# Kernel optimization log

Measured on AMD Instinct MI355X. Metric: run time of the kernel, lower is better.

Reference implementation:

```python
import jax, jax.numpy as jnp
import numpy as np

N, E, B = 20000, 200000, 16
ND, ED, GD, HD, DOF = 64, 32, 32, 128, 6
PI = 3.14159265358979

def _hat(v):
    x, y, z = v[..., 0], v[..., 1], v[..., 2]
    O = jnp.zeros_like(x)
    return jnp.stack([jnp.stack([O, -z, y], -1),
                      jnp.stack([z, O, -x], -1),
                      jnp.stack([-y, x, O], -1)], -2)

def _so3_exp(phi):
    th2 = jnp.sum(phi * phi, -1, keepdims=True)
    th = jnp.sqrt(th2 + 1e-12)
    a = jnp.where(th < 1e-4, 1.0 - th2 / 6.0, jnp.sin(th) / th)
    b = jnp.where(th < 1e-4, 0.5 - th2 / 24.0, (1.0 - jnp.cos(th)) / th2)
    K = _hat(phi)
    I = jnp.eye(3, dtype=phi.dtype)
    return I + a[..., None] * K + b[..., None] * (K @ K)

def _se3_exp(rho, phi):
    # returns (R, t) of Exp([rho, phi]) with rotation part phi
    th2 = jnp.sum(phi * phi, -1, keepdims=True)
    th = jnp.sqrt(th2 + 1e-12)
    a = jnp.where(th < 1e-4, 1.0 - th2 / 6.0, jnp.sin(th) / th)
    b = jnp.where(th < 1e-4, 0.5 - th2 / 24.0, (1.0 - jnp.cos(th)) / th2)
    c = jnp.where(th < 1e-4, 1.0 / 6.0 - th2 / 120.0, (th - jnp.sin(th)) / (th2 * th))
    K = _hat(phi)
    KK = K @ K
    I = jnp.eye(3, dtype=phi.dtype)
    R = I + a[..., None] * K + b[..., None] * KK
    V = I + b[..., None] * K + c[..., None] * KK
    t = jnp.einsum('nij,nj->ni', V, rho)
    return R, t

def _comp(Ra, ta, Rb, tb):
    return Ra @ Rb, jnp.einsum('nij,nj->ni', Ra, tb) + ta

def _inv(R, t):
    Rt = jnp.swapaxes(R, -1, -2)
    return Rt, -jnp.einsum('nij,nj->ni', Rt, t)

def _vec(R, t):
    # flattened [R | t] 3x4 -> 12
    return jnp.concatenate([R, t[..., None]], -1).reshape(R.shape[0], 12)

def setup_inputs() -> dict:
    key = jax.random.key(0)
    ks = jax.random.split(key, 16)
    T_R = _so3_exp(0.5 * jax.random.normal(ks[0], (N, 3)))
    Tij_R = _so3_exp(0.5 * jax.random.normal(ks[1], (E, 3)))
    return {
        'xfeat': jax.random.normal(ks[2], (N, ND), jnp.float32),
        'T_R': T_R.astype(jnp.float32),
        'T_t': jax.random.normal(ks[3], (N, 3), jnp.float32),
        'edge_feat': jax.random.normal(ks[4], (E, ED), jnp.float32),
        'Tij_R': Tij_R.astype(jnp.float32),
        'Tij_t': jax.random.normal(ks[5], (E, 3), jnp.float32),
        'u': jax.random.normal(ks[6], (B, GD), jnp.float32),
        'edge_index': jax.random.randint(ks[7], (2, E), 0, N),
        'batch': jnp.sort(jax.random.randint(ks[8], (N,), 0, B)),
        'W1': 0.05 * jax.random.normal(ks[9], (2 * ND + 12 + ED, HD), jnp.float32),
        'b1': jnp.zeros((HD,), jnp.float32),
        'W2': 0.05 * jax.random.normal(ks[10], (HD, HD), jnp.float32),
        'b2': jnp.zeros((HD,), jnp.float32),
        'W3': 0.05 * jax.random.normal(ks[11], (HD + GD + ND, HD), jnp.float32),
        'b3': jnp.zeros((HD,), jnp.float32),
        'W4': 0.05 * jax.random.normal(ks[12], (HD, ND + DOF), jnp.float32),
        'b4': jnp.zeros((ND + DOF,), jnp.float32),
    }

def reference(xfeat, T_R, T_t, edge_feat, Tij_R, Tij_t, u,
              edge_index, batch, W1, b1, W2, b2, W3, b3, W4, b4):
    n = xfeat.shape[0]
    i, j = edge_index[0], edge_index[1]
    xfi, xfj = xfeat[i], xfeat[j]
    Ri, ti = T_R[i], T_t[i]
    Rj, tj = T_R[j], T_t[j]
    # T_err_ij = Tj * Ti.inv() * Tij_hat.inv()
    Rii, tii = _inv(Ri, ti)
    Ra, ta = _comp(Rj, tj, Rii, tii)
    Rhi, thi = _inv(Tij_R, Tij_t)
    Reij, teij = _comp(Ra, ta, Rhi, thi)
    # T_err_ji = Ti * Tj.inv() * Tij_hat
    Rji_, tji_ = _inv(Rj, tj)
    Rb, tb = _comp(Ri, ti, Rji_, tji_)
    Reji, teji = _comp(Rb, tb, Tij_R, Tij_t)
    f_ij = jnp.concatenate([xfi, xfj, edge_feat, _vec(Reij, teij)], 1)
    f_ji = jnp.concatenate([xfj, xfi, edge_feat, _vec(Reji, teji)], 1)
    feats = jnp.concatenate([f_ij, f_ji], 0)          # [2E, 172]
    j_both = jnp.concatenate([j, i], 0)               # [2E]
    h = jax.nn.relu(feats @ W1 + b1)
    h = jax.nn.relu(h @ W2 + b2)                      # [2E, HD]
    sums = jax.ops.segment_sum(h, j_both, num_segments=n)
    cnt = jax.ops.segment_sum(jnp.ones((h.shape[0], 1), h.dtype), j_both, num_segments=n)
    aggr = sums / jnp.maximum(cnt, 1.0)               # scatter_mean
    g = jnp.concatenate([aggr, xfeat, u[batch]], 1)
    out = jax.nn.relu(g @ W3 + b3) @ W4 + b4
    xupd, tupd = out[:, :-DOF], out[:, -DOF:]
    rho, phi = tupd[:, :3], tupd[:, 3:]
    # SquashRot: bound rotation angle to pi via tanh
    th = jnp.linalg.norm(phi, axis=-1, keepdims=True)
    phi = phi * (PI * jnp.tanh(th / PI) / (th + 1e-8))
    Rd, td = _se3_exp(rho, phi)
    R_out, t_out = _comp(Rd, td, T_R, T_t)            # boxplus_left: Exp(d) * T
    xfeat_out = xfeat + xupd
    theta = jnp.linalg.norm(phi, axis=-1, keepdims=True)
    return jnp.concatenate([xfeat_out, R_out.reshape(n, 9), t_out, theta], -1)
```

## Files before the change

### kernel.cpp

```cpp
#include <hip/hip_runtime.h>
#include <math.h>

#define ND 64
#define ED 32
#define GD 32
#define HD 128
#define DOF 6
#define K1 172
#define K1PAD 192
#define KG 224
#define N4P 80
#define NOUT 70
#define OUTC 77
#define MT 256
#define P1 144
#define TDN 16
#define GP 232
#define HP 136
#define OP 84
#define PI_F 3.14159265358979f

typedef short short8 __attribute__((ext_vector_type(8)));
typedef float f32x4  __attribute__((ext_vector_type(4)));

__device__ __forceinline__ unsigned short f2b(float f) {
    unsigned int u = __float_as_uint(f);
    u += 0x7fffu + ((u >> 16) & 1u);
    return (unsigned short)(u >> 16);
}
__device__ __forceinline__ float b2f(unsigned short b) {
    return __uint_as_float(((unsigned int)b) << 16);
}
__device__ __forceinline__ void mul33_abt(const float* A, const float* B, float* C) {
#pragma unroll
    for (int r = 0; r < 3; r++)
#pragma unroll
        for (int c = 0; c < 3; c++)
            C[3*r+c] = A[3*r+0]*B[3*c+0] + A[3*r+1]*B[3*c+1] + A[3*r+2]*B[3*c+2];
}

__global__ void __launch_bounds__(256)
prep(const float* __restrict__ W1, const float* __restrict__ W2,
     const float* __restrict__ W3, const float* __restrict__ W4,
     const float* __restrict__ xfeat, const float* __restrict__ edge_feat,
     unsigned short* __restrict__ W1b, unsigned short* __restrict__ W2b,
     unsigned short* __restrict__ W3b, unsigned short* __restrict__ W4b,
     unsigned short* __restrict__ xb, unsigned short* __restrict__ eb,
     int N, int E)
{
    int idx = blockIdx.x * 256 + threadIdx.x;
    if (idx < K1PAD * HD) {
        int k = idx >> 7, n = idx & 127;
        float v = (k < K1) ? W1[k * HD + n] : 0.f;
        int kc = k >> 5, kr = k & 31, q = kr >> 3, j = kr & 7;
        W1b[(((kc * 8 + (n >> 4)) * 4 + q) * 16 + (n & 15)) * 8 + j] = f2b(v);
        return;
    }
    idx -= K1PAD * HD;
    if (idx < HD * HD) {
        int k = idx >> 7, n = idx & 127;
        int kc = k >> 5, kr = k & 31, q = kr >> 3, j = kr & 7;
        W2b[(((kc * 8 + (n >> 4)) * 4 + q) * 16 + (n & 15)) * 8 + j] = f2b(W2[k * HD + n]);
        return;
    }
    idx -= HD * HD;
    if (idx < KG * HD) {
        int k = idx >> 7, n = idx & 127;
        int sk = (k < HD) ? ((k & 7) * 16 + (k >> 3)) : k;
        int kc = k >> 5, kr = k & 31, q = kr >> 3, j = kr & 7;
        W3b[(((kc * 8 + (n >> 4)) * 4 + q) * 16 + (n & 15)) * 8 + j] = f2b(W3[sk * HD + n]);
        return;
    }
    idx -= KG * HD;
    if (idx < HD * N4P) {
        int k = idx / N4P, n = idx % N4P;
        float v = (n < NOUT) ? W4[k * NOUT + n] : 0.f;
        int kc = k >> 5, kr = k & 31, q = kr >> 3, j = kr & 7;
        W4b[(((kc * 5 + (n >> 4)) * 4 + q) * 16 + (n & 15)) * 8 + j] = f2b(v);
        return;
    }
    idx -= HD * N4P;
    const int nx4 = N * ND / 4;
    if (idx < nx4) {
        const float4 v = *(const float4*)&xfeat[idx * 4];
        ushort4 o; o.x = f2b(v.x); o.y = f2b(v.y); o.z = f2b(v.z); o.w = f2b(v.w);
        *(ushort4*)&xb[idx * 4] = o;
        return;
    }
    idx -= nx4;
    if (idx < E * ED / 4) {
        const float4 v = *(const float4*)&edge_feat[idx * 4];
        ushort4 o; o.x = f2b(v.x); o.y = f2b(v.y); o.z = f2b(v.z); o.w = f2b(v.w);
        *(ushort4*)&eb[idx * 4] = o;
    }
}

__global__ void __launch_bounds__(256)
count_kernel(const int* __restrict__ edge_index, int* __restrict__ cnti, int E)
{
    int g = blockIdx.x * 256 + threadIdx.x;
    if (g >= 2 * E) return;
    const int tgt = (g < E) ? edge_index[E + g] : edge_index[g - E];
    atomicAdd(&cnti[tgt], 1);
}

__global__ void __launch_bounds__(1024)
scan_kernel(const int* __restrict__ cnti, int* __restrict__ off,
            int* __restrict__ cursor, int N)
{
    __shared__ int part[1024];
    const int t = threadIdx.x;
    const int chunk = (N + 1023) / 1024;
    const int base = t * chunk;
    int s = 0;
    for (int i = 0; i < chunk; i++) { int idx = base + i; if (idx < N) s += cnti[idx]; }
    part[t] = s;
    __syncthreads();
    for (int d = 1; d < 1024; d <<= 1) {
        int v = (t >= d) ? part[t - d] : 0;
        __syncthreads();
        part[t] += v;
        __syncthreads();
    }
    int pre = (t > 0) ? part[t - 1] : 0;
    for (int i = 0; i < chunk; i++) {
        int idx = base + i;
        if (idx < N) { off[idx] = pre; cursor[idx] = pre; pre += cnti[idx]; }
    }
}

__global__ void __launch_bounds__(256)
scatter_kernel(const int* __restrict__ edge_index, int* __restrict__ cursor,
               int* __restrict__ dlist, int E)
{
    int g = blockIdx.x * 256 + threadIdx.x;
    if (g >= 2 * E) return;
    const int tgt = (g < E) ? edge_index[E + g] : edge_index[g - E];
    const int pos = atomicAdd(&cursor[tgt], 1);
    dlist[pos] = g;
}

__global__ void __launch_bounds__(256)
pose_kernel(const float* __restrict__ T_R, const float* __restrict__ T_t,
            const float* __restrict__ Tij_R, const float* __restrict__ Tij_t,
            const int* __restrict__ edge_index, const int* __restrict__ dlist,
            unsigned short* __restrict__ poseb, int E)
{
    const int p = blockIdx.x * 256 + threadIdx.x;
    if (p >= 2 * E) return;
    const int dir = dlist[p];
    const bool fwd = (dir < E);
    const int e = fwd ? dir : dir - E;
    const int ni = edge_index[e];
    const int nj = edge_index[E + e];
    float Ri[9], Rj[9], TR[9], ti[3], tj[3], Tt[3];
#pragma unroll
    for (int q = 0; q < 9; q++) { Ri[q] = T_R[9*ni+q]; Rj[q] = T_R[9*nj+q]; TR[q] = Tij_R[9*e+q]; }
#pragma unroll
    for (int q = 0; q < 3; q++) { ti[q] = T_t[3*ni+q]; tj[q] = T_t[3*nj+q]; Tt[q] = Tij_t[3*e+q]; }
    float A[9];
    mul33_abt(Rj, Ri, A);
    float Re[9], te[3];
    if (fwd) {
        mul33_abt(A, TR, Re);
#pragma unroll
        for (int r = 0; r < 3; r++)
            te[r] = tj[r]
                  - (A[3*r+0]*ti[0] + A[3*r+1]*ti[1] + A[3*r+2]*ti[2])
                  - (Re[3*r+0]*Tt[0] + Re[3*r+1]*Tt[1] + Re[3*r+2]*Tt[2]);
    } else {
#pragma unroll
        for (int r = 0; r < 3; r++)
#pragma unroll
            for (int c = 0; c < 3; c++)
                Re[3*r+c] = A[r]*TR[c] + A[3+r]*TR[3+c] + A[6+r]*TR[6+c];
        const float d0 = Tt[0]-tj[0], d1 = Tt[1]-tj[1], d2 = Tt[2]-tj[2];
#pragma unroll
        for (int r = 0; r < 3; r++)
            te[r] = ti[r] + A[r]*d0 + A[3+r]*d1 + A[6+r]*d2;
    }
    short8 p0, p1;
#pragma unroll
    for (int r = 0; r < 2; r++) {
        p0[4*r+0] = (short)f2b(Re[3*r+0]);
        p0[4*r+1] = (short)f2b(Re[3*r+1]);
        p0[4*r+2] = (short)f2b(Re[3*r+2]);
        p0[4*r+3] = (short)f2b(te[r]);
    }
    p1[0] = (short)f2b(Re[6]); p1[1] = (short)f2b(Re[7]);
    p1[2] = (short)f2b(Re[8]); p1[3] = (short)f2b(te[2]);
    p1[4] = 0; p1[5] = 0; p1[6] = 0; p1[7] = 0;
    *(short8*)(poseb + (size_t)p * 16) = p0;
    *(short8*)(poseb + (size_t)p * 16 + 8) = p1;
}

__global__ void __launch_bounds__(256, 2)
edge_kernel(const unsigned short* __restrict__ xb, const unsigned short* __restrict__ eb,
            const unsigned short* __restrict__ poseb, const int* __restrict__ edge_index,
            const int* __restrict__ dlist,
            const unsigned short* __restrict__ W1b, const float* __restrict__ b1,
            const unsigned short* __restrict__ W2b, const float* __restrict__ b2,
            unsigned short* __restrict__ hbuf, int E)
{
    __shared__ unsigned short h1s[4 * 64 * P1];
    const int tid = threadIdx.x;
    const int wv = tid >> 6, lane = tid & 63;
    const int nl = lane & 15, quad = lane >> 4;
    const int D0 = blockIdx.x * MT + wv * 64;
    const int laneoff = quad * 128 + nl * 8;
    const int twoE = 2 * E;
    unsigned short* hw = h1s + wv * 64 * P1;

    int s1[4], s2[4], ee[4], pp[4];
#pragma unroll
    for (int rt = 0; rt < 4; rt++) {
        int p = D0 + rt * 16 + nl;
        if (p >= twoE) p = twoE - 1;
        pp[rt] = p;
        const int dir = dlist[p];
        const bool fwd = (dir < E);
        const int e = fwd ? dir : dir - E;
        const int ni = edge_index[e];
        const int nj = edge_index[E + e];
        s1[rt] = fwd ? ni : nj;
        s2[rt] = fwd ? nj : ni;
        ee[rt] = e;
    }

    f32x4 acc[4][8];
#pragma unroll
    for (int rt = 0; rt < 4; rt++)
#pragma unroll
        for (int nt = 0; nt < 8; nt++) acc[rt][nt] = (f32x4)0.f;

    short8 wf[2][8];
#pragma unroll
    for (int nt = 0; nt < 8; nt++)
        wf[0][nt] = *(const short8*)(W1b + nt * 512 + laneoff);

#pragma unroll
    for (int kc = 0; kc < 6; kc++) {
        short8 af[4];
#pragma unroll
        for (int rt = 0; rt < 4; rt++) {
            switch (kc) {
            case 0: af[rt] = *(const short8*)(xb + (size_t)s1[rt] * ND + quad * 8); break;
            case 1: af[rt] = *(const short8*)(xb + (size_t)s1[rt] * ND + 32 + quad * 8); break;
            case 2: af[rt] = *(const short8*)(xb + (size_t)s2[rt] * ND + quad * 8); break;
            case 3: af[rt] = *(const short8*)(xb + (size_t)s2[rt] * ND + 32 + quad * 8); break;
            case 4: af[rt] = *(const short8*)(eb + (size_t)ee[rt] * ED + quad * 8); break;
            default: af[rt] = (quad < 2) ? *(const short8*)(poseb + (size_t)pp[rt] * 16 + quad * 8)
                                         : (short8)(short)0; break;
            }
        }
        const int cur = kc & 1, nxt = cur ^ 1;
        if (kc < 5) {
#pragma unroll
            for (int nt = 0; nt < 8; nt++)
                wf[nxt][nt] = *(const short8*)(W1b + ((kc + 1) * 8 + nt) * 512 + laneoff);
        }
#pragma unroll
        for (int nt = 0; nt < 8; nt++)
#pragma unroll
            for (int rt = 0; rt < 4; rt++)
                acc[rt][nt] = __builtin_amdgcn_mfma_f32_16x16x32_bf16(af[rt], wf[cur][nt], acc[rt][nt], 0, 0, 0);
    }

    {
        float bias1[8];
#pragma unroll
        for (int nt = 0; nt < 8; nt++) bias1[nt] = b1[nt * 16 + nl];
#pragma unroll
        for (int rt = 0; rt < 4; rt++)
#pragma unroll
            for (int nt = 0; nt < 8; nt++) {
                const int col = nt * 16 + nl;
#pragma unroll
                for (int r = 0; r < 4; r++)
                    hw[(rt * 16 + quad * 4 + r) * P1 + col] = f2b(fmaxf(acc[rt][nt][r] + bias1[nt], 0.f));
            }
    }
    asm volatile("s_waitcnt lgkmcnt(0)" ::: "memory");

#pragma unroll
    for (int rt = 0; rt < 4; rt++)
#pragma unroll
        for (int nt = 0; nt < 8; nt++) acc[rt][nt] = (f32x4)0.f;
#pragma unroll
    for (int nt = 0; nt < 8; nt++)
        wf[0][nt] = *(const short8*)(W2b + nt * 512 + laneoff);
#pragma unroll
    for (int kc = 0; kc < 4; kc++) {
        short8 hf[4];
#pragma unroll
        for (int rt = 0; rt < 4; rt++)
            hf[rt] = *(const short8*)&hw[(rt * 16 + nl) * P1 + kc * 32 + quad * 8];
        const int cur = kc & 1, nxt = cur ^ 1;
        if (kc < 3) {
#pragma unroll
            for (int nt = 0; nt < 8; nt++)
                wf[nxt][nt] = *(const short8*)(W2b + ((kc + 1) * 8 + nt) * 512 + laneoff);
        }
#pragma unroll
        for (int nt = 0; nt < 8; nt++)
#pragma unroll
            for (int rt = 0; rt < 4; rt++)
                acc[rt][nt] = __builtin_amdgcn_mfma_f32_16x16x32_bf16(hf[rt], wf[cur][nt], acc[rt][nt], 0, 0, 0);
    }

    {
        float bias2[8];
#pragma unroll
        for (int nt = 0; nt < 8; nt++) bias2[nt] = b2[nt * 16 + nl];
#pragma unroll
        for (int rt = 0; rt < 4; rt++)
#pragma unroll
            for (int r = 0; r < 4; r++) {
                const int p2 = D0 + rt * 16 + quad * 4 + r;
                if (p2 < twoE) {
                    short8 hv;
#pragma unroll
                    for (int nt = 0; nt < 8; nt++)
                        hv[nt] = (short)f2b(fmaxf(acc[rt][nt][r] + bias2[nt], 0.f));
                    *(short8*)(hbuf + (size_t)p2 * HD + nl * 8) = hv;
                }
            }
    }
}

__global__ void __launch_bounds__(256)
node_kernel(const float* __restrict__ xfeat, const float* __restrict__ T_R,
            const float* __restrict__ T_t, const float* __restrict__ u,
            const int* __restrict__ batch,
            const unsigned short* __restrict__ W3b, const float* __restrict__ b3,
            const unsigned short* __restrict__ W4b, const float* __restrict__ b4,
            const unsigned short* __restrict__ hbuf, const int* __restrict__ off,
            const int* __restrict__ cnti,
            float* __restrict__ out, int Nn)
{
    __shared__ unsigned short gbuf[TDN * GP];
    __shared__ unsigned short hid[TDN * HP];
    __shared__ float obuf[TDN * OP];
    const int tid = threadIdx.x;
    const int wv = tid >> 6, lane = tid & 63;
    const int n0 = blockIdx.x * TDN;
    const int nn = min(TDN, Nn - n0);

#pragma unroll
    for (int i = 0; i < 4; i++) {
        const int d = wv + 4 * i;
        if (d < nn) {
            const int n = n0 + d;
            const int deg = cnti[n];
            const int start = off[n];
            const float inv = 1.0f / (float)max(deg, 1);
            const unsigned short* hp = hbuf + (size_t)start * HD + 2 * lane;
            float a0 = 0.f, a1 = 0.f;
            int k = 0;
            for (; k + 4 <= deg; k += 4) {
                const unsigned int v0 = *(const unsigned int*)(hp);
                const unsigned int v1 = *(const unsigned int*)(hp + HD);
                const unsigned int v2 = *(const unsigned int*)(hp + 2 * HD);
                const unsigned int v3 = *(const unsigned int*)(hp + 3 * HD);
                hp += 4 * HD;
                a0 += b2f((unsigned short)v0) + b2f((unsigned short)v1)
                    + b2f((unsigned short)v2) + b2f((unsigned short)v3);
                a1 += b2f((unsigned short)(v0 >> 16)) + b2f((unsigned short)(v1 >> 16))
                    + b2f((unsigned short)(v2 >> 16)) + b2f((unsigned short)(v3 >> 16));
            }
            for (; k < deg; k++) {
                const unsigned int v0 = *(const unsigned int*)(hp);
                hp += HD;
                a0 += b2f((unsigned short)v0);
                a1 += b2f((unsigned short)(v0 >> 16));
            }
            const unsigned int pk = (unsigned int)f2b(a0 * inv) | ((unsigned int)f2b(a1 * inv) << 16);
            *(unsigned int*)&gbuf[d * GP + 2 * lane] = pk;
        }
    }
    for (int idx = tid; idx < TDN * 24; idx += 256) {
        const int d = idx / 24;
        if (d < nn) {
            const int n = n0 + d;
            const int c4 = (idx % 24) * 4;
            float4 v;
            if (c4 < 64) v = *(const float4*)&xfeat[(size_t)n * ND + c4];
            else         v = *(const float4*)&u[(size_t)batch[n] * GD + (c4 - 64)];
            ushort4 o; o.x = f2b(v.x); o.y = f2b(v.y); o.z = f2b(v.z); o.w = f2b(v.w);
            *(ushort4*)&gbuf[d * GP + 128 + c4] = o;
        }
    }
    __syncthreads();

    const int nl = lane & 15, quad = lane >> 4;
    const int laneoff = quad * 128 + nl * 8;

    f32x4 acc3[2];
    acc3[0] = (f32x4)0.f; acc3[1] = (f32x4)0.f;
#pragma unroll
    for (int kc = 0; kc < 7; kc++) {
        short8 A0 = *(const short8*)&gbuf[nl * GP + kc * 32 + quad * 8];
#pragma unroll
        for (int t = 0; t < 2; t++) {
            short8 B = *(const short8*)(W3b + (kc * 8 + wv * 2 + t) * 512 + laneoff);
            acc3[t] = __builtin_amdgcn_mfma_f32_16x16x32_bf16(A0, B, acc3[t], 0, 0, 0);
        }
    }
#pragma unroll
    for (int t = 0; t < 2; t++) {
        const int col = (wv * 2 + t) * 16 + nl;
        const float bb = b3[col];
#pragma unroll
        for (int r = 0; r < 4; r++)
            hid[(quad * 4 + r) * HP + col] = f2b(fmaxf(acc3[t][r] + bb, 0.f));
    }
    __syncthreads();

    f32x4 acc4[2];
    acc4[0] = (f32x4)0.f; acc4[1] = (f32x4)0.f;
    const int nt1 = (wv == 0) ? 4 : -1;
#pragma unroll
    for (int kc = 0; kc < 4; kc++) {
        short8 A0 = *(const short8*)&hid[nl * HP + kc * 32 + quad * 8];
        short8 B0 = *(const short8*)(W4b + (kc * 5 + wv) * 512 + laneoff);
        acc4[0] = __builtin_amdgcn_mfma_f32_16x16x32_bf16(A0, B0, acc4[0], 0, 0, 0);
        if (nt1 >= 0) {
            short8 B1 = *(const short8*)(W4b + (kc * 5 + nt1) * 512 + laneoff);
            acc4[1] = __builtin_amdgcn_mfma_f32_16x16x32_bf16(A0, B1, acc4[1], 0, 0, 0);
        }
    }
    {
        const int col0 = wv * 16 + nl;
        const float bb0 = (col0 < NOUT) ? b4[col0] : 0.f;
#pragma unroll
        for (int r = 0; r < 4; r++)
            obuf[(quad * 4 + r) * OP + col0] = acc4[0][r] + bb0;
        if (nt1 >= 0) {
            const int col1 = nt1 * 16 + nl;
            const float bb1 = (col1 < NOUT) ? b4[col1] : 0.f;
#pragma unroll
            for (int r = 0; r < 4; r++)
                obuf[(quad * 4 + r) * OP + col1] = acc4[1][r] + bb1;
        }
    }
    __syncthreads();

    for (int idx = tid; idx < TDN * ND; idx += 256) {
        const int d = idx >> 6, c = idx & 63;
        if (d < nn) {
            const int n = n0 + d;
            out[(size_t)n * OUTC + c] = xfeat[(size_t)n * ND + c] + obuf[d * OP + c];
        }
    }
    if (tid < nn) {
        const int n = n0 + tid;
        const float r0 = obuf[tid*OP + 64], r1 = obuf[tid*OP + 65], r2 = obuf[tid*OP + 66];
        float p0 = obuf[tid*OP + 67], p1 = obuf[tid*OP + 68], p2 = obuf[tid*OP + 69];
        const float th0 = sqrtf(p0*p0 + p1*p1 + p2*p2);
        const float s = PI_F * tanhf(th0 / PI_F) / (th0 + 1e-8f);
        p0 *= s; p1 *= s; p2 *= s;
        const float pp = p0*p0 + p1*p1 + p2*p2;
        const float th = sqrtf(pp + 1e-12f);
        float a, b, c;
        if (th < 1e-4f) { a = 1.f - pp/6.f; b = 0.5f - pp/24.f; c = 1.f/6.f - pp/120.f; }
        else { const float sn = sinf(th), cs = cosf(th); a = sn/th; b = (1.f-cs)/pp; c = (th-sn)/(pp*th); }
        float Rd[9], V[9];
        Rd[0]=1.f+b*(p0*p0-pp); Rd[1]=-a*p2+b*p0*p1; Rd[2]= a*p1+b*p0*p2;
        Rd[3]= a*p2+b*p1*p0;    Rd[4]=1.f+b*(p1*p1-pp); Rd[5]=-a*p0+b*p1*p2;
        Rd[6]=-a*p1+b*p2*p0;    Rd[7]= a*p0+b*p2*p1;  Rd[8]=1.f+b*(p2*p2-pp);
        V[0]=1.f+c*(p0*p0-pp);  V[1]=-b*p2+c*p0*p1;   V[2]= b*p1+c*p0*p2;
        V[3]= b*p2+c*p1*p0;     V[4]=1.f+c*(p1*p1-pp); V[5]=-b*p0+c*p1*p2;
        V[6]=-b*p1+c*p2*p0;     V[7]= b*p0+c*p2*p1;   V[8]=1.f+c*(p2*p2-pp);
        const float td0 = V[0]*r0 + V[1]*r1 + V[2]*r2;
        const float td1 = V[3]*r0 + V[4]*r1 + V[5]*r2;
        const float td2 = V[6]*r0 + V[7]*r1 + V[8]*r2;
        float TRn[9], Ttn[3];
#pragma unroll
        for (int q = 0; q < 9; q++) TRn[q] = T_R[9*n+q];
#pragma unroll
        for (int q = 0; q < 3; q++) Ttn[q] = T_t[3*n+q];
        float* o = out + (size_t)n * OUTC + 64;
#pragma unroll
        for (int r = 0; r < 3; r++)
#pragma unroll
            for (int cc = 0; cc < 3; cc++)
                o[3*r+cc] = Rd[3*r+0]*TRn[cc] + Rd[3*r+1]*TRn[3+cc] + Rd[3*r+2]*TRn[6+cc];
        o[9]  = Rd[0]*Ttn[0] + Rd[1]*Ttn[1] + Rd[2]*Ttn[2] + td0;
        o[10] = Rd[3]*Ttn[0] + Rd[4]*Ttn[1] + Rd[5]*Ttn[2] + td1;
        o[11] = Rd[6]*Ttn[0] + Rd[7]*Ttn[1] + Rd[8]*Ttn[2] + td2;
        o[12] = sqrtf(pp);
    }
}

extern "C" void kernel_launch(void* const* d_in, const int* in_sizes, int n_in,
                              void* d_out, int out_size, void* d_ws, size_t ws_size,
                              hipStream_t stream)
{
    const float* xfeat     = (const float*)d_in[0];
    const float* T_R       = (const float*)d_in[1];
    const float* T_t       = (const float*)d_in[2];
    const float* edge_feat = (const float*)d_in[3];
    const float* Tij_R     = (const float*)d_in[4];
    const float* Tij_t     = (const float*)d_in[5];
    const float* u         = (const float*)d_in[6];
    const int*   edge_index= (const int*)d_in[7];
    const int*   batch     = (const int*)d_in[8];
    const float* W1 = (const float*)d_in[9],  *b1 = (const float*)d_in[10];
    const float* W2 = (const float*)d_in[11], *b2 = (const float*)d_in[12];
    const float* W3 = (const float*)d_in[13], *b3 = (const float*)d_in[14];
    const float* W4 = (const float*)d_in[15], *b4 = (const float*)d_in[16];
    const int N = in_sizes[0] / ND;
    const int E = in_sizes[3] / ED;

    char* p = (char*)d_ws;
    unsigned short* W1b = (unsigned short*)p;   p += (size_t)K1PAD * HD * 2;
    unsigned short* W2b = (unsigned short*)p;   p += (size_t)HD * HD * 2;
    unsigned short* W3b = (unsigned short*)p;   p += (size_t)KG * HD * 2;
    unsigned short* W4b = (unsigned short*)p;   p += (size_t)HD * N4P * 2;
    unsigned short* xb  = (unsigned short*)p;   p += (size_t)N * ND * 2;
    unsigned short* ebf = (unsigned short*)p;   p += (size_t)E * ED * 2;
    unsigned short* poseb = (unsigned short*)p; p += (size_t)2 * E * 16 * 2;
    unsigned short* hbuf = (unsigned short*)p;  p += (size_t)2 * E * HD * 2;
    int* dlist = (int*)p;                       p += (size_t)2 * E * 4;
    int* cnti = (int*)p;                        p += (size_t)N * 4;
    int* off  = (int*)p;                        p += (size_t)N * 4;
    int* cursor = (int*)p;

    hipMemsetAsync(cnti, 0, (size_t)N * 4, stream);
    const int prepn = K1PAD*HD + HD*HD + KG*HD + HD*N4P + N*ND/4 + E*ED/4;
    prep<<<(prepn + 255) / 256, 256, 0, stream>>>(W1, W2, W3, W4, xfeat, edge_feat,
                                                  W1b, W2b, W3b, W4b, xb, ebf, N, E);
    count_kernel<<<(2*E + 255) / 256, 256, 0, stream>>>(edge_index, cnti, E);
    scan_kernel<<<1, 1024, 0, stream>>>(cnti, off, cursor, N);
    scatter_kernel<<<(2*E + 255) / 256, 256, 0, stream>>>(edge_index, cursor, dlist, E);
    pose_kernel<<<(2*E + 255) / 256, 256, 0, stream>>>(T_R, T_t, Tij_R, Tij_t,
                                                       edge_index, dlist, poseb, E);
    const int ebk = (2 * E + MT - 1) / MT;
    edge_kernel<<<ebk, 256, 0, stream>>>(xb, ebf, poseb, edge_index, dlist,
                                         W1b, b1, W2b, b2, hbuf, E);
    const int nb = (N + TDN - 1) / TDN;
    node_kernel<<<nb, 256, 0, stream>>>(xfeat, T_R, T_t, u, batch, W3b, b3, W4b, b4,
                                        hbuf, off, cnti, (float*)d_out, N);
}
```

Baseline: 324.2 us.

## Fuse count into prep, scatter with pose, prefetch A operands, transpose MFMA output

```diff
diff --git a/kernel.cpp b/kernel.cpp
--- a/kernel.cpp
+++ b/kernel.cpp
@@ -13,11 +13,12 @@
 #define NOUT 70
 #define OUTC 77
 #define MT 256
-#define P1 144
+#define P1 136
 #define TDN 16
 #define GP 232
 #define HP 136
 #define OP 84
+#define NMAX 20480
 #define PI_F 3.14159265358979f
 
 typedef short short8 __attribute__((ext_vector_type(8)));
@@ -43,10 +44,11 @@
 prep(const float* __restrict__ W1, const float* __restrict__ W2,
      const float* __restrict__ W3, const float* __restrict__ W4,
      const float* __restrict__ xfeat, const float* __restrict__ edge_feat,
+     const int* __restrict__ edge_index,
      unsigned short* __restrict__ W1b, unsigned short* __restrict__ W2b,
      unsigned short* __restrict__ W3b, unsigned short* __restrict__ W4b,
      unsigned short* __restrict__ xb, unsigned short* __restrict__ eb,
-     int N, int E)
+     int* __restrict__ cnti, int N, int E)
 {
     int idx = blockIdx.x * 256 + threadIdx.x;
     if (idx < K1PAD * HD) {
@@ -88,32 +90,33 @@
         return;
     }
     idx -= nx4;
-    if (idx < E * ED / 4) {
+    const int ne4 = E * ED / 4;
+    if (idx < ne4) {
         const float4 v = *(const float4*)&edge_feat[idx * 4];
         ushort4 o; o.x = f2b(v.x); o.y = f2b(v.y); o.z = f2b(v.z); o.w = f2b(v.w);
         *(ushort4*)&eb[idx * 4] = o;
-    }
-}
-
-__global__ void __launch_bounds__(256)
-count_kernel(const int* __restrict__ edge_index, int* __restrict__ cnti, int E)
-{
-    int g = blockIdx.x * 256 + threadIdx.x;
-    if (g >= 2 * E) return;
-    const int tgt = (g < E) ? edge_index[E + g] : edge_index[g - E];
-    atomicAdd(&cnti[tgt], 1);
+        return;
+    }
+    idx -= ne4;
+    if (idx < 2 * E) {
+        const int tgt = (idx < E) ? edge_index[E + idx] : edge_index[idx - E];
+        atomicAdd(&cnti[tgt], 1);
+    }
 }
 
 __global__ void __launch_bounds__(1024)
 scan_kernel(const int* __restrict__ cnti, int* __restrict__ off,
             int* __restrict__ cursor, int N)
 {
+    __shared__ int sh[NMAX];
     __shared__ int part[1024];
     const int t = threadIdx.x;
+    for (int i = t; i < N; i += 1024) sh[i] = cnti[i];
+    __syncthreads();
     const int chunk = (N + 1023) / 1024;
     const int base = t * chunk;
     int s = 0;
-    for (int i = 0; i < chunk; i++) { int idx = base + i; if (idx < N) s += cnti[idx]; }
+    for (int i = 0; i < chunk; i++) { int idx = base + i; if (idx < N) s += sh[idx]; }
     part[t] = s;
     __syncthreads();
     for (int d = 1; d < 1024; d <<= 1) {
@@ -125,34 +128,28 @@
     int pre = (t > 0) ? part[t - 1] : 0;
     for (int i = 0; i < chunk; i++) {
         int idx = base + i;
-        if (idx < N) { off[idx] = pre; cursor[idx] = pre; pre += cnti[idx]; }
-    }
+        if (idx < N) { int c = sh[idx]; sh[idx] = pre; pre += c; }
+    }
+    __syncthreads();
+    for (int i = t; i < N; i += 1024) { off[i] = sh[i]; cursor[i] = sh[i]; }
 }
 
 __global__ void __launch_bounds__(256)
-scatter_kernel(const int* __restrict__ edge_index, int* __restrict__ cursor,
-               int* __restrict__ dlist, int E)
+scatter_pose(const float* __restrict__ T_R, const float* __restrict__ T_t,
+             const float* __restrict__ Tij_R, const float* __restrict__ Tij_t,
+             const int* __restrict__ edge_index, int* __restrict__ cursor,
+             int4* __restrict__ dinfo, unsigned short* __restrict__ poseb, int E)
 {
-    int g = blockIdx.x * 256 + threadIdx.x;
+    const int g = blockIdx.x * 256 + threadIdx.x;
     if (g >= 2 * E) return;
-    const int tgt = (g < E) ? edge_index[E + g] : edge_index[g - E];
-    const int pos = atomicAdd(&cursor[tgt], 1);
-    dlist[pos] = g;
-}
-
-__global__ void __launch_bounds__(256)
-pose_kernel(const float* __restrict__ T_R, const float* __restrict__ T_t,
-            const float* __restrict__ Tij_R, const float* __restrict__ Tij_t,
-            const int* __restrict__ edge_index, const int* __restrict__ dlist,
-            unsigned short* __restrict__ poseb, int E)
-{
-    const int p = blockIdx.x * 256 + threadIdx.x;
-    if (p >= 2 * E) return;
-    const int dir = dlist[p];
-    const bool fwd = (dir < E);
-    const int e = fwd ? dir : dir - E;
+    const bool fwd = (g < E);
+    const int e = fwd ? g : g - E;
     const int ni = edge_index[e];
     const int nj = edge_index[E + e];
+    const int tgt = fwd ? nj : ni;
+    const int pos = atomicAdd(&cursor[tgt], 1);
+    dinfo[pos] = make_int4(fwd ? ni : nj, fwd ? nj : ni, e, g);
+
     float Ri[9], Rj[9], TR[9], ti[3], tj[3], Tt[3];
 #pragma unroll
     for (int q = 0; q < 9; q++) { Ri[q] = T_R[9*ni+q]; Rj[q] = T_R[9*nj+q]; TR[q] = Tij_R[9*e+q]; }
@@ -190,14 +187,13 @@
     p1[0] = (short)f2b(Re[6]); p1[1] = (short)f2b(Re[7]);
     p1[2] = (short)f2b(Re[8]); p1[3] = (short)f2b(te[2]);
     p1[4] = 0; p1[5] = 0; p1[6] = 0; p1[7] = 0;
-    *(short8*)(poseb + (size_t)p * 16) = p0;
-    *(short8*)(poseb + (size_t)p * 16 + 8) = p1;
+    *(short8*)(poseb + (size_t)pos * 16) = p0;
+    *(short8*)(poseb + (size_t)pos * 16 + 8) = p1;
 }
 
 __global__ void __launch_bounds__(256, 2)
 edge_kernel(const unsigned short* __restrict__ xb, const unsigned short* __restrict__ eb,
-            const unsigned short* __restrict__ poseb, const int* __restrict__ edge_index,
-            const int* __restrict__ dlist,
+            const unsigned short* __restrict__ poseb, const int4* __restrict__ dinfo,
             const unsigned short* __restrict__ W1b, const float* __restrict__ b1,
             const unsigned short* __restrict__ W2b, const float* __restrict__ b2,
             unsigned short* __restrict__ hbuf, int E)
@@ -217,68 +213,62 @@
         int p = D0 + rt * 16 + nl;
         if (p >= twoE) p = twoE - 1;
         pp[rt] = p;
-        const int dir = dlist[p];
-        const bool fwd = (dir < E);
-        const int e = fwd ? dir : dir - E;
-        const int ni = edge_index[e];
-        const int nj = edge_index[E + e];
-        s1[rt] = fwd ? ni : nj;
-        s2[rt] = fwd ? nj : ni;
-        ee[rt] = e;
+        const int4 di = dinfo[p];
+        s1[rt] = di.x; s2[rt] = di.y; ee[rt] = di.z;
     }
 
     f32x4 acc[4][8];
 #pragma unroll
     for (int rt = 0; rt < 4; rt++)
 #pragma unroll
-        for (int nt = 0; nt < 8; nt++) acc[rt][nt] = (f32x4)0.f;
-
-    short8 wf[2][8];
+        for (int At = 0; At < 8; At++) acc[rt][At] = (f32x4)0.f;
+
+    short8 af[2][4], wf[2][8];
+#pragma unroll
+    for (int rt = 0; rt < 4; rt++)
+        af[0][rt] = *(const short8*)(xb + (size_t)s1[rt] * ND + quad * 8);
 #pragma unroll
     for (int nt = 0; nt < 8; nt++)
         wf[0][nt] = *(const short8*)(W1b + nt * 512 + laneoff);
 
 #pragma unroll
     for (int kc = 0; kc < 6; kc++) {
-        short8 af[4];
-#pragma unroll
-        for (int rt = 0; rt < 4; rt++) {
-            switch (kc) {
-            case 0: af[rt] = *(const short8*)(xb + (size_t)s1[rt] * ND + quad * 8); break;
-            case 1: af[rt] = *(const short8*)(xb + (size_t)s1[rt] * ND + 32 + quad * 8); break;
-            case 2: af[rt] = *(const short8*)(xb + (size_t)s2[rt] * ND + quad * 8); break;
-            case 3: af[rt] = *(const short8*)(xb + (size_t)s2[rt] * ND + 32 + quad * 8); break;
-            case 4: af[rt] = *(const short8*)(eb + (size_t)ee[rt] * ED + quad * 8); break;
-            default: af[rt] = (quad < 2) ? *(const short8*)(poseb + (size_t)pp[rt] * 16 + quad * 8)
-                                         : (short8)(short)0; break;
-            }
-        }
         const int cur = kc & 1, nxt = cur ^ 1;
         if (kc < 5) {
 #pragma unroll
+            for (int rt = 0; rt < 4; rt++) {
+                switch (kc + 1) {
+                case 1: af[nxt][rt] = *(const short8*)(xb + (size_t)s1[rt] * ND + 32 + quad * 8); break;
+                case 2: af[nxt][rt] = *(const short8*)(xb + (size_t)s2[rt] * ND + quad * 8); break;
+                case 3: af[nxt][rt] = *(const short8*)(xb + (size_t)s2[rt] * ND + 32 + quad * 8); break;
+                case 4: af[nxt][rt] = *(const short8*)(eb + (size_t)ee[rt] * ED + quad * 8); break;
+                default: af[nxt][rt] = (quad < 2) ? *(const short8*)(poseb + (size_t)pp[rt] * 16 + quad * 8)
+                                                  : (short8)(short)0; break;
+                }
+            }
+#pragma unroll
             for (int nt = 0; nt < 8; nt++)
                 wf[nxt][nt] = *(const short8*)(W1b + ((kc + 1) * 8 + nt) * 512 + laneoff);
         }
 #pragma unroll
-        for (int nt = 0; nt < 8; nt++)
+        for (int At = 0; At < 8; At++)
 #pragma unroll
             for (int rt = 0; rt < 4; rt++)
-                acc[rt][nt] = __builtin_amdgcn_mfma_f32_16x16x32_bf16(af[rt], wf[cur][nt], acc[rt][nt], 0, 0, 0);
-    }
-
-    {
-        float bias1[8];
-#pragma unroll
-        for (int nt = 0; nt < 8; nt++) bias1[nt] = b1[nt * 16 + nl];
-#pragma unroll
-        for (int rt = 0; rt < 4; rt++)
-#pragma unroll
-            for (int nt = 0; nt < 8; nt++) {
-                const int col = nt * 16 + nl;
-#pragma unroll
-                for (int r = 0; r < 4; r++)
-                    hw[(rt * 16 + quad * 4 + r) * P1 + col] = f2b(fmaxf(acc[rt][nt][r] + bias1[nt], 0.f));
-            }
+                acc[rt][At] = __builtin_amdgcn_mfma_f32_16x16x32_bf16(wf[cur][At], af[cur][rt], acc[rt][At], 0, 0, 0);
+    }
+
+#pragma unroll
+    for (int At = 0; At < 8; At++) {
+        const f32x4 bv = *(const f32x4*)&b1[At * 16 + quad * 4];
+#pragma unroll
+        for (int rt = 0; rt < 4; rt++) {
+            unsigned int lo = (unsigned int)f2b(fmaxf(acc[rt][At][0] + bv[0], 0.f))
+                            | ((unsigned int)f2b(fmaxf(acc[rt][At][1] + bv[1], 0.f)) << 16);
+            unsigned int hi = (unsigned int)f2b(fmaxf(acc[rt][At][2] + bv[2], 0.f))
+                            | ((unsigned int)f2b(fmaxf(acc[rt][At][3] + bv[3], 0.f)) << 16);
+            uint2 pk; pk.x = lo; pk.y = hi;
+            *(uint2*)&hw[(rt * 16 + nl) * P1 + At * 16 + quad * 4] = pk;
+        }
     }
     asm volatile("s_waitcnt lgkmcnt(0)" ::: "memory");
 
@@ -521,22 +511,21 @@
     unsigned short* ebf = (unsigned short*)p;   p += (size_t)E * ED * 2;
     unsigned short* poseb = (unsigned short*)p; p += (size_t)2 * E * 16 * 2;
     unsigned short* hbuf = (unsigned short*)p;  p += (size_t)2 * E * HD * 2;
-    int* dlist = (int*)p;                       p += (size_t)2 * E * 4;
+    int4* dinfo = (int4*)p;                     p += (size_t)2 * E * 16;
     int* cnti = (int*)p;                        p += (size_t)N * 4;
     int* off  = (int*)p;                        p += (size_t)N * 4;
     int* cursor = (int*)p;
 
     hipMemsetAsync(cnti, 0, (size_t)N * 4, stream);
-    const int prepn = K1PAD*HD + HD*HD + KG*HD + HD*N4P + N*ND/4 + E*ED/4;
+    const int prepn = K1PAD*HD + HD*HD + KG*HD + HD*N4P + N*ND/4 + E*ED/4 + 2*E;
     prep<<<(prepn + 255) / 256, 256, 0, stream>>>(W1, W2, W3, W4, xfeat, edge_feat,
-                                                  W1b, W2b, W3b, W4b, xb, ebf, N, E);
-    count_kernel<<<(2*E + 255) / 256, 256, 0, stream>>>(edge_index, cnti, E);
+                                                  edge_index, W1b, W2b, W3b, W4b,
+                                                  xb, ebf, cnti, N, E);
     scan_kernel<<<1, 1024, 0, stream>>>(cnti, off, cursor, N);
-    scatter_kernel<<<(2*E + 255) / 256, 256, 0, stream>>>(edge_index, cursor, dlist, E);
-    pose_kernel<<<(2*E + 255) / 256, 256, 0, stream>>>(T_R, T_t, Tij_R, Tij_t,
-                                                       edge_index, dlist, poseb, E);
+    scatter_pose<<<(2*E + 255) / 256, 256, 0, stream>>>(T_R, T_t, Tij_R, Tij_t,
+                                                        edge_index, cursor, dinfo, poseb, E);
     const int ebk = (2 * E + MT - 1) / MT;
-    edge_kernel<<<ebk, 256, 0, stream>>>(xb, ebf, poseb, edge_index, dlist,
+    edge_kernel<<<ebk, 256, 0, stream>>>(xb, ebf, poseb, dinfo,
                                          W1b, b1, W2b, b2, hbuf, E);
     const int nb = (N + TDN - 1) / TDN;
     node_kernel<<<nb, 256, 0, stream>>>(xfeat, T_R, T_t, u, batch, W3b, b3, W4b, b4,
```

Result: faster. 266.0 us (-18.0%).
